# Performance work log

Measured on AMD Instinct MI355X. Metric: run time of the kernel, lower is better.

Reference implementation:

```python
import jax, jax.numpy as jnp
import numpy as np

D_MODEL = 1024
NUM_HEAD = 16
D_K = D_MODEL // NUM_HEAD


def setup_inputs() -> dict:
    key = jax.random.key(0)
    ks = jax.random.split(key, 11)
    B, S = 2, 2048
    s = 1.0 / np.sqrt(D_MODEL)
    return {
        "q": jax.random.normal(ks[0], (B, S, D_MODEL), jnp.float32),
        "k": jax.random.normal(ks[1], (B, S, D_MODEL), jnp.float32),
        "v": jax.random.normal(ks[2], (B, S, D_MODEL), jnp.float32),
        "Wq": jax.random.normal(ks[3], (D_MODEL, D_MODEL), jnp.float32) * s,
        "bq": jnp.zeros((D_MODEL,), jnp.float32),
        "Wk": jax.random.normal(ks[4], (D_MODEL, D_MODEL), jnp.float32) * s,
        "bk": jnp.zeros((D_MODEL,), jnp.float32),
        "Wv": jax.random.normal(ks[5], (D_MODEL, D_MODEL), jnp.float32) * s,
        "bv": jnp.zeros((D_MODEL,), jnp.float32),
        "Wo": jax.random.normal(ks[6], (D_MODEL, D_MODEL), jnp.float32) * s,
        "bo": jnp.zeros((D_MODEL,), jnp.float32),
    }


def _split_head(x, B):
    # [B, S, d_model] -> [B, H, S, d_k]
    S = x.shape[1]
    return x.reshape(B, S, NUM_HEAD, D_K).transpose(0, 2, 1, 3)


def reference(q, k, v, Wq, bq, Wk, bk, Wv, bv, Wo, bo):
    B = q.shape[0]
    qh = _split_head(q @ Wq + bq, B)  # [B,H,Sq,dk]
    kh = _split_head(k @ Wk + bk, B)  # [B,H,Sk,dk]
    vh = _split_head(v @ Wv + bv, B)  # [B,H,Sk,dk]
    scores = jnp.einsum("bhqd,bhkd->bhqk", qh, kh) / jnp.sqrt(
        jnp.asarray(D_K, qh.dtype)
    )
    attn = jax.nn.softmax(scores, axis=-1)
    out = jnp.einsum("bhqk,bhkd->bhqd", attn, vh)  # [B,H,Sq,dk]
    out = out.transpose(0, 2, 1, 3).reshape(B, -1, D_MODEL)
    return jax.nn.relu(out @ Wo + bo)
```

## Files before the change

kernel.cpp:

```cpp
#include <hip/hip_runtime.h>
#include <math.h>

#define SEQ 2048
#define NHD 16

typedef float f32x4 __attribute__((ext_vector_type(4), may_alias));
typedef _Float16 h16x8 __attribute__((ext_vector_type(8), may_alias));
typedef _Float16 h16x4 __attribute__((ext_vector_type(4), may_alias));

__device__ __forceinline__ void gl_lds16(const void* g, void* l) {
  __builtin_amdgcn_global_load_lds(
      (const __attribute__((address_space(1))) unsigned int*)g,
      (__attribute__((address_space(3))) unsigned int*)l, 16, 0, 0);
}

struct PrepArgs {
  const float* W[4];
  _Float16* T[4];
  const float* X[3];
  _Float16* H[3];
};

__global__ __launch_bounds__(256) void prep_k(PrepArgs a) {
  __shared__ float tile[64][65];
  const int blk = blockIdx.x;
  const int t = threadIdx.x;
  if (blk < 1024) {
    const int widx = blk >> 8, tl = blk & 255;
    const int nb = (tl & 15) * 64, kb = (tl >> 4) * 64;
    const float* __restrict__ W = a.W[widx];
    _Float16* __restrict__ T = a.T[widx];
    const int c = t & 63, r0 = t >> 6;
#pragma unroll
    for (int i = 0; i < 16; ++i) {
      const int r = i * 4 + r0;
      tile[r][c] = W[(size_t)(kb + r) * 1024 + nb + c];
    }
    __syncthreads();
#pragma unroll
    for (int i = 0; i < 16; ++i) {
      const int n = i * 4 + r0;
      T[(size_t)(nb + n) * 1024 + kb + c] = (_Float16)tile[c][n];
    }
  } else {
    const int b2 = blk - 1024;
    const int z = b2 >> 11, bx = b2 & 2047;
    const float* __restrict__ X = a.X[z];
    _Float16* __restrict__ H = a.H[z];
    const size_t i = ((size_t)bx * 256 + t) * 8;
    const f32x4 f0 = *(const f32x4*)(X + i);
    const f32x4 f1 = *(const f32x4*)(X + i + 4);
    const float fs[8] = {f0.x, f0.y, f0.z, f0.w, f1.x, f1.y, f1.z, f1.w};
    h16x8 o;
#pragma unroll
    for (int j = 0; j < 8; ++j) o[j] = (_Float16)fs[j];
    *(h16x8*)(H + i) = o;
  }
}

__global__ __launch_bounds__(256) void vtrans_k(const unsigned short* __restrict__ Vb,
                                                unsigned short* __restrict__ Vt) {
  __shared__ unsigned short tile[64][65];
  const int t = threadIdx.x;
  const int c = t & 63, r0 = t >> 6;
  const int s0 = blockIdx.x * 64;
  const int bh = blockIdx.y;
#pragma unroll
  for (int i = 0; i < 16; ++i) {
    const int r = i * 4 + r0;
    tile[r][c] = Vb[((size_t)bh * SEQ + s0 + r) * 64 + c];
  }
  __syncthreads();
#pragma unroll
  for (int i = 0; i < 16; ++i) {
    const int d = i * 4 + r0;
    const int sp = ((c & 15) * 4) + (c >> 4);
    Vt[((size_t)bh * 64 + d) * SEQ + s0 + sp] = tile[c][d];
  }
}

struct QKVArgs {
  const _Float16* A[3];
  const _Float16* Bt[3];
  const float* bias[3];
  _Float16* C[3];
};

__global__ __launch_bounds__(256, 4) void gemm_qkv_k(QKVArgs a) {
  __shared__ char smem[32768];
  const int dblk = blockIdx.x;
  const int z = dblk >> 8;
  const int rb = dblk & 255;
  const int n0 = ((rb >> 3) & 7) * 128;
  const int m0 = ((((rb >> 6) << 3) | (rb & 7))) * 128;
  const _Float16* __restrict__ A = a.A[z];
  const _Float16* __restrict__ Bt = a.Bt[z];
  const float* __restrict__ bias = a.bias[z];
  _Float16* __restrict__ C = a.C[z];

  const int t = threadIdx.x;
  const int l = t & 63, w = t >> 6;
  const int quad = l >> 4, l15 = l & 15;
  const int wm = w >> 1, wn = w & 1;

  auto stage = [&](int buf, int k0) {
#pragma unroll
    for (int it = 0; it < 2; ++it) {
      const int c = it * 4 + w;
      const int rr = c * 16 + l15;
      gl_lds16(A + (size_t)(m0 + rr) * 1024 + k0 + quad * 8,
               smem + buf * 16384 + c * 1024);
      gl_lds16(Bt + (size_t)(n0 + rr) * 1024 + k0 + quad * 8,
               smem + buf * 16384 + 8192 + c * 1024);
    }
  };

  const f32x4 z4 = {0.f, 0.f, 0.f, 0.f};
  f32x4 acc[4][4];
#pragma unroll
  for (int i = 0; i < 4; ++i)
#pragma unroll
    for (int j = 0; j < 4; ++j) acc[i][j] = z4;

  stage(0, 0);
  __syncthreads();
  int cur = 0;
  for (int k0 = 0; k0 < 1024; k0 += 32) {
    if (k0 + 32 < 1024) stage(cur ^ 1, k0 + 32);
    const h16x8* lds8 = (const h16x8*)(smem + cur * 16384);
    h16x8 af[4], bf[4];
#pragma unroll
    for (int i = 0; i < 4; ++i) {
      af[i] = lds8[(wm * 4 + i) * 64 + l];
      bf[i] = lds8[512 + (wn * 4 + i) * 64 + l];
    }
#pragma unroll
    for (int i = 0; i < 4; ++i)
#pragma unroll
      for (int j = 0; j < 4; ++j)
        acc[i][j] = __builtin_amdgcn_mfma_f32_16x16x32_f16(af[i], bf[j], acc[i][j], 0, 0, 0);
    __syncthreads();
    cur ^= 1;
  }
#pragma unroll
  for (int i = 0; i < 4; ++i)
#pragma unroll
    for (int j = 0; j < 4; ++j) {
      const int col = n0 + wn * 64 + j * 16 + l15;
      const float bv = bias[col];
#pragma unroll
      for (int r = 0; r < 4; ++r) {
        const int row = m0 + wm * 64 + i * 16 + quad * 4 + r;
        const int b = row >> 11, s = row & 2047;
        const int h = col >> 6, d = col & 63;
        C[((size_t)(b * NHD + h) * SEQ + s) * 64 + d] = (_Float16)(acc[i][j][r] + bv);
      }
    }
}

__global__ __launch_bounds__(256) void gemm_o_k(
    const _Float16* __restrict__ Op0, const _Float16* __restrict__ Op1,
    const float* __restrict__ Lp, const _Float16* __restrict__ Bt,
    const float* __restrict__ bias, float* __restrict__ Cf) {
  __shared__ char smem[40960];
  float* inv_lds = (float*)(smem + 32768);
  const int rb = blockIdx.x;
  const int n0 = ((rb >> 3) & 7) * 128;
  const int m0 = ((((rb >> 6) << 3) | (rb & 7))) * 128;
  const int t = threadIdx.x;
  const int l = t & 63, w = t >> 6;
  const int quad = l >> 4, l15 = l & 15;
  const int wm = w >> 1, wn = w & 1;
  const int arow0 = t >> 2, aq = t & 3;

#pragma unroll
  for (int e = t; e < 2048; e += 256) {
    const int rl = e >> 4, hh = e & 15;
    const int m = m0 + rl;
    const int b = m >> 11, s = m & 2047;
    const size_t li = (size_t)(b * NHD + hh) * 2048 + s;
    inv_lds[e] = 1.f / (Lp[li] + Lp[65536 + li]);
  }
  __syncthreads();

  auto stageB = [&](int buf, int k0) {
#pragma unroll
    for (int it = 0; it < 2; ++it) {
      const int c = it * 4 + w;
      const int rr = c * 16 + l15;
      gl_lds16(Bt + (size_t)(n0 + rr) * 1024 + k0 + quad * 8,
               smem + buf * 8192 + c * 1024);
    }
  };
  auto loadA = [&](int k0, h16x8 (&r0)[2], h16x8 (&r1)[2]) {
#pragma unroll
    for (int it = 0; it < 2; ++it) {
      const size_t off = (size_t)(m0 + it * 64 + arow0) * 1024 + k0 + aq * 8;
      r0[it] = *(const h16x8*)(Op0 + off);
      r1[it] = *(const h16x8*)(Op1 + off);
    }
  };
  auto writeA = [&](int buf, int k0, const h16x8 (&r0)[2], const h16x8 (&r1)[2]) {
    const int head = k0 >> 6;
    h16x8* alds = (h16x8*)(smem + 16384 + buf * 8192);
#pragma unroll
    for (int it = 0; it < 2; ++it) {
      const int row = it * 64 + arow0;
      const int slot = (row >> 4) * 64 + aq * 16 + ((row & 15) ^ (aq * 2));
      const float inv = inv_lds[row * 16 + head];
      h16x8 hv;
#pragma unroll
      for (int j = 0; j < 8; ++j)
        hv[j] = (_Float16)(((float)r0[it][j] + (float)r1[it][j]) * inv);
      alds[slot] = hv;
    }
  };

  const f32x4 z4 = {0.f, 0.f, 0.f, 0.f};
  f32x4 acc[4][4];
#pragma unroll
  for (int i = 0; i < 4; ++i)
#pragma unroll
    for (int j = 0; j < 4; ++j) acc[i][j] = z4;

  h16x8 a0r[2], a1r[2];
  loadA(0, a0r, a1r);
  stageB(0, 0);
  writeA(0, 0, a0r, a1r);
  __syncthreads();
  int cur = 0;
  for (int k0 = 0; k0 < 1024; k0 += 32) {
    const int nk = k0 + 32;
    if (nk < 1024) {
      loadA(nk, a0r, a1r);
      stageB(cur ^ 1, nk);
    }
    const h16x8* blds = (const h16x8*)(smem + cur * 8192);
    const h16x8* alds = (const h16x8*)(smem + 16384 + cur * 8192);
    h16x8 af[4], bf[4];
#pragma unroll
    for (int i = 0; i < 4; ++i) {
      af[i] = alds[(wm * 4 + i) * 64 + quad * 16 + (l15 ^ (quad * 2))];
      bf[i] = blds[(wn * 4 + i) * 64 + l];
    }
#pragma unroll
    for (int i = 0; i < 4; ++i)
#pragma unroll
      for (int j = 0; j < 4; ++j)
        acc[i][j] = __builtin_amdgcn_mfma_f32_16x16x32_f16(af[i], bf[j], acc[i][j], 0, 0, 0);
    if (nk < 1024) writeA(cur ^ 1, nk, a0r, a1r);
    __syncthreads();
    cur ^= 1;
  }
#pragma unroll
  for (int i = 0; i < 4; ++i)
#pragma unroll
    for (int j = 0; j < 4; ++j) {
      const int col = n0 + wn * 64 + j * 16 + l15;
      const float bv = bias[col];
#pragma unroll
      for (int r = 0; r < 4; ++r) {
        const int row = m0 + wm * 64 + i * 16 + quad * 4 + r;
        Cf[(size_t)row * 1024 + col] = fmaxf(acc[i][j][r] + bv, 0.f);
      }
    }
}

__global__ __launch_bounds__(256, 4) void attn_k(
    const _Float16* __restrict__ Qf, const _Float16* __restrict__ Kf,
    const _Float16* __restrict__ Vtp,
    _Float16* __restrict__ Op0, _Float16* __restrict__ Op1,
    float* __restrict__ Lp) {
  __shared__ char smem[34816];
  h16x8* lds8 = (h16x8*)smem;
  const int dblk = blockIdx.x;
  const int comb = ((dblk >> 7) << 3) | (dblk & 7);
  const int q0 = ((dblk >> 3) & 15) * 128;
  const int bh = comb >> 1;
  const int kz = comb & 1;
  const int t = threadIdx.x;
  const int l = t & 63, w = t >> 6;
  const int quad = l >> 4, l15 = l & 15;
  const int b = bh >> 4, h = bh & 15;

  const _Float16* Kb = Kf + (size_t)bh * SEQ * 64;
  const _Float16* Vtb = Vtp + (size_t)bh * 64 * SEQ;

  h16x8 qf[2][2];
#pragma unroll
  for (int mi = 0; mi < 2; ++mi) {
    const size_t qb = ((size_t)bh * SEQ + q0 + w * 32 + mi * 16 + l15) * 64;
#pragma unroll
    for (int ks = 0; ks < 2; ++ks)
      qf[mi][ks] = *(const h16x8*)&Qf[qb + ks * 32 + quad * 8];
  }
  const f32x4 z4 = {0.f, 0.f, 0.f, 0.f};
  f32x4 oacc[2][4], lacc[2];
#pragma unroll
  for (int mi = 0; mi < 2; ++mi) {
    lacc[mi] = z4;
#pragma unroll
    for (int i = 0; i < 4; ++i) oacc[mi][i] = z4;
  }
  h16x8 ones;
#pragma unroll
  for (int j = 0; j < 8; ++j) ones[j] = (_Float16)1.0f;

  const int kbeg = kz * 1024;
  for (int k0 = kbeg; k0 < kbeg + 1024; k0 += 64) {
#pragma unroll
    for (int it = 0; it < 2; ++it) {
      const int c = it * 4 + w;
      const int kd = (c >> 1) * 16 + l15;
      const int off2 = (c & 1) * 32 + quad * 8;
      gl_lds16(Kb + (size_t)(k0 + kd) * 64 + off2, smem + c * 1024);
      gl_lds16(Vtb + (size_t)kd * SEQ + k0 + off2, smem + 8192 + c * 1024);
    }
    __syncthreads();

    {
      h16x8 kfr[4][2];
#pragma unroll
      for (int nt = 0; nt < 4; ++nt)
#pragma unroll
        for (int ks = 0; ks < 2; ++ks) kfr[nt][ks] = lds8[(nt * 2 + ks) * 64 + l];

#pragma unroll
      for (int mi = 0; mi < 2; ++mi) {
        f32x4 sacc[4];
#pragma unroll
        for (int nt = 0; nt < 4; ++nt) {
          f32x4 s = z4;
          s = __builtin_amdgcn_mfma_f32_16x16x32_f16(qf[mi][0], kfr[nt][0], s, 0, 0, 0);
          s = __builtin_amdgcn_mfma_f32_16x16x32_f16(qf[mi][1], kfr[nt][1], s, 0, 0, 0);
          sacc[nt] = s;
        }
        char* pb = smem + 16384 + (w * 2 + mi) * 2304;
#pragma unroll
        for (int r = 0; r < 4; ++r) {
          h16x4 pk;
#pragma unroll
          for (int nt = 0; nt < 4; ++nt)
            pk[nt] = (_Float16)__expf(sacc[nt][r] * 0.125f);
          *(h16x4*)(pb + (quad * 4 + r) * 144 + l15 * 8) = pk;
        }
      }
    }
    __asm__ __volatile__("" ::: "memory");

    {
      h16x8 vfr[4][2];
#pragma unroll
      for (int nt = 0; nt < 4; ++nt)
#pragma unroll
        for (int ks = 0; ks < 2; ++ks) vfr[nt][ks] = lds8[512 + (nt * 2 + ks) * 64 + l];

#pragma unroll
      for (int mi = 0; mi < 2; ++mi) {
        char* pb = smem + 16384 + (w * 2 + mi) * 2304;
        const h16x8 pf0 = *(const h16x8*)(pb + l15 * 144 + quad * 16);
        const h16x8 pf1 = *(const h16x8*)(pb + l15 * 144 + 64 + quad * 16);
        lacc[mi] = __builtin_amdgcn_mfma_f32_16x16x32_f16(pf0, ones, lacc[mi], 0, 0, 0);
        lacc[mi] = __builtin_amdgcn_mfma_f32_16x16x32_f16(pf1, ones, lacc[mi], 0, 0, 0);
#pragma unroll
        for (int nt = 0; nt < 4; ++nt) {
          oacc[mi][nt] = __builtin_amdgcn_mfma_f32_16x16x32_f16(pf0, vfr[nt][0], oacc[mi][nt], 0, 0, 0);
          oacc[mi][nt] = __builtin_amdgcn_mfma_f32_16x16x32_f16(pf1, vfr[nt][1], oacc[mi][nt], 0, 0, 0);
        }
      }
    }
    __syncthreads();
  }

  _Float16* __restrict__ Op = kz ? Op1 : Op0;
#pragma unroll
  for (int mi = 0; mi < 2; ++mi)
#pragma unroll
    for (int nt = 0; nt < 4; ++nt)
#pragma unroll
      for (int r = 0; r < 4; ++r) {
        const size_t tok = (size_t)b * SEQ + q0 + w * 32 + mi * 16 + quad * 4 + r;
        Op[tok * 1024 + h * 64 + nt * 16 + l15] = (_Float16)oacc[mi][nt][r];
      }
  if (l15 == 0) {
#pragma unroll
    for (int mi = 0; mi < 2; ++mi)
#pragma unroll
      for (int r = 0; r < 4; ++r) {
        const int row = q0 + w * 32 + mi * 16 + quad * 4 + r;
        Lp[(size_t)kz * 65536 + bh * 2048 + row] = lacc[mi][r];
      }
  }
}

extern "C" void kernel_launch(void* const* d_in, const int* in_sizes, int n_in,
                              void* d_out, int out_size, void* d_ws, size_t ws_size,
                              hipStream_t stream) {
  const float* q = (const float*)d_in[0];
  const float* k = (const float*)d_in[1];
  const float* v = (const float*)d_in[2];
  const float* Wq = (const float*)d_in[3];
  const float* bq = (const float*)d_in[4];
  const float* Wk = (const float*)d_in[5];
  const float* bk = (const float*)d_in[6];
  const float* Wv = (const float*)d_in[7];
  const float* bv = (const float*)d_in[8];
  const float* Wo = (const float*)d_in[9];
  const float* bo = (const float*)d_in[10];

  char* W8 = (char*)d_ws;
  const size_t MB = 1024 * 1024;
  auto F = [&](size_t off) { return (_Float16*)(W8 + off); };
  _Float16* wt[4] = {F(0), F(2 * MB), F(4 * MB), F(6 * MB)};
  _Float16* qf = F(8 * MB);
  _Float16* kf = F(16 * MB);
  _Float16* vf = F(24 * MB);
  _Float16* Qf = F(32 * MB);
  _Float16* Kf = F(40 * MB);
  _Float16* Vb = F(48 * MB);
  _Float16* Vt = F(56 * MB);
  _Float16* Op0 = F(8 * MB);
  _Float16* Op1 = F(16 * MB);
  float* Lp = (float*)(W8 + 64 * MB);

  const dim3 blk(256);

  PrepArgs pa;
  pa.W[0] = Wq; pa.W[1] = Wk; pa.W[2] = Wv; pa.W[3] = Wo;
  pa.T[0] = wt[0]; pa.T[1] = wt[1]; pa.T[2] = wt[2]; pa.T[3] = wt[3];
  pa.X[0] = q; pa.X[1] = k; pa.X[2] = v;
  pa.H[0] = qf; pa.H[1] = kf; pa.H[2] = vf;
  prep_k<<<dim3(7168), blk, 0, stream>>>(pa);

  QKVArgs qa;
  qa.A[0] = qf; qa.A[1] = kf; qa.A[2] = vf;
  qa.Bt[0] = wt[0]; qa.Bt[1] = wt[1]; qa.Bt[2] = wt[2];
  qa.bias[0] = bq; qa.bias[1] = bk; qa.bias[2] = bv;
  qa.C[0] = Qf; qa.C[1] = Kf; qa.C[2] = Vb;
  gemm_qkv_k<<<dim3(768), blk, 0, stream>>>(qa);

  vtrans_k<<<dim3(32, 32), blk, 0, stream>>>((const unsigned short*)Vb,
                                             (unsigned short*)Vt);
  attn_k<<<dim3(1024), blk, 0, stream>>>(Qf, Kf, Vt, Op0, Op1, Lp);
  gemm_o_k<<<dim3(256), blk, 0, stream>>>(Op0, Op1, Lp, wt[3], bo, (float*)d_out);
}
```

Measured before the change: 254.4 us.

## Enlarge QKV GEMM tiles to 256x256 with 512 threads and swizzled LDS

Rewrites the fused QKV projection GEMM to use 256x256 output tiles with 8 waves per block, a K-step of 64, and 128 KB of double-buffered LDS. An XOR swizzle is applied to the LDS layout to avoid bank conflicts, and explicit vmcnt waits plus raw barriers replace __syncthreads. The goal is more data reuse per LDS load and fewer global loads per MFMA. In exchange only 192 blocks are launched, which may underfill the GPU's CUs, and each thread holds a larger accumulator set, so register pressure rises.

```diff
diff --git a/kernel.cpp b/kernel.cpp
--- a/kernel.cpp
+++ b/kernel.cpp
@@ -86,13 +86,13 @@
   _Float16* C[3];
 };
 
-__global__ __launch_bounds__(256, 4) void gemm_qkv_k(QKVArgs a) {
-  __shared__ char smem[32768];
+__global__ __launch_bounds__(512, 2) void gemm_qkv_k(QKVArgs a) {
+  __shared__ __align__(16) char smem[131072];
   const int dblk = blockIdx.x;
-  const int z = dblk >> 8;
-  const int rb = dblk & 255;
-  const int n0 = ((rb >> 3) & 7) * 128;
-  const int m0 = ((((rb >> 6) << 3) | (rb & 7))) * 128;
+  const int z = dblk >> 6;
+  const int rb = dblk & 63;
+  const int m0 = (rb >> 2) * 256;
+  const int n0 = (rb & 3) * 256;
   const _Float16* __restrict__ A = a.A[z];
   const _Float16* __restrict__ Bt = a.Bt[z];
   const float* __restrict__ bias = a.bias[z];
@@ -101,59 +101,86 @@
   const int t = threadIdx.x;
   const int l = t & 63, w = t >> 6;
   const int quad = l >> 4, l15 = l & 15;
-  const int wm = w >> 1, wn = w & 1;
-
-  auto stage = [&](int buf, int k0) {
-#pragma unroll
-    for (int it = 0; it < 2; ++it) {
-      const int c = it * 4 + w;
-      const int rr = c * 16 + l15;
-      gl_lds16(A + (size_t)(m0 + rr) * 1024 + k0 + quad * 8,
-               smem + buf * 16384 + c * 1024);
-      gl_lds16(Bt + (size_t)(n0 + rr) * 1024 + k0 + quad * 8,
-               smem + buf * 16384 + 8192 + c * 1024);
+  const int wm = w >> 2, wn = w & 3;
+
+  const int srow = t >> 3;
+  const int sslot = (t & 7) ^ (srow & 7);
+  size_t goffA[4], goffB[4];
+#pragma unroll
+  for (int j = 0; j < 4; ++j) {
+    goffA[j] = (size_t)(m0 + j * 64 + srow) * 1024 + sslot * 8;
+    goffB[j] = (size_t)(n0 + j * 64 + srow) * 1024 + sslot * 8;
+  }
+
+  auto stage = [&](int buf, int kt) {
+    const int k0 = kt * 64;
+    char* base = smem + buf * 65536;
+#pragma unroll
+    for (int j = 0; j < 4; ++j) {
+      gl_lds16(A + goffA[j] + k0, base + j * 8192 + w * 1024);
+      gl_lds16(Bt + goffB[j] + k0, base + 32768 + j * 8192 + w * 1024);
     }
   };
 
   const f32x4 z4 = {0.f, 0.f, 0.f, 0.f};
-  f32x4 acc[4][4];
-#pragma unroll
-  for (int i = 0; i < 4; ++i)
+  f32x4 acc[8][4];
+#pragma unroll
+  for (int i = 0; i < 8; ++i)
 #pragma unroll
     for (int j = 0; j < 4; ++j) acc[i][j] = z4;
 
+  const int xr = l15 & 7;
+
   stage(0, 0);
-  __syncthreads();
-  int cur = 0;
-  for (int k0 = 0; k0 < 1024; k0 += 32) {
-    if (k0 + 32 < 1024) stage(cur ^ 1, k0 + 32);
-    const h16x8* lds8 = (const h16x8*)(smem + cur * 16384);
-    h16x8 af[4], bf[4];
-#pragma unroll
-    for (int i = 0; i < 4; ++i) {
-      af[i] = lds8[(wm * 4 + i) * 64 + l];
-      bf[i] = lds8[512 + (wn * 4 + i) * 64 + l];
-    }
-#pragma unroll
-    for (int i = 0; i < 4; ++i)
-#pragma unroll
-      for (int j = 0; j < 4; ++j)
-        acc[i][j] = __builtin_amdgcn_mfma_f32_16x16x32_f16(af[i], bf[j], acc[i][j], 0, 0, 0);
-    __syncthreads();
-    cur ^= 1;
-  }
-#pragma unroll
-  for (int i = 0; i < 4; ++i)
-#pragma unroll
-    for (int j = 0; j < 4; ++j) {
-      const int col = n0 + wn * 64 + j * 16 + l15;
+  for (int kt = 0; kt < 16; ++kt) {
+    const int cur = kt & 1;
+    if (kt < 15) {
+      stage(cur ^ 1, kt + 1);
+      asm volatile("s_waitcnt vmcnt(8)" ::: "memory");
+    } else {
+      asm volatile("s_waitcnt vmcnt(0)" ::: "memory");
+    }
+    __builtin_amdgcn_sched_barrier(0);
+    __builtin_amdgcn_s_barrier();
+
+    const char* base = smem + cur * 65536;
+    h16x8 bf[4][2];
+#pragma unroll
+    for (int nj = 0; nj < 4; ++nj) {
+      const int rowB = wn * 64 + nj * 16 + l15;
+#pragma unroll
+      for (int h = 0; h < 2; ++h) {
+        const int sl = (h * 4 + quad) ^ xr;
+        bf[nj][h] = *(const h16x8*)(base + 32768 + rowB * 128 + sl * 16);
+      }
+    }
+#pragma unroll
+    for (int mi = 0; mi < 8; ++mi) {
+      const int rowA = wm * 128 + mi * 16 + l15;
+      const h16x8 af0 = *(const h16x8*)(base + rowA * 128 + ((quad ^ xr) * 16));
+      const h16x8 af1 = *(const h16x8*)(base + rowA * 128 + (((4 + quad) ^ xr) * 16));
+#pragma unroll
+      for (int nj = 0; nj < 4; ++nj) {
+        acc[mi][nj] = __builtin_amdgcn_mfma_f32_16x16x32_f16(af0, bf[nj][0], acc[mi][nj], 0, 0, 0);
+        acc[mi][nj] = __builtin_amdgcn_mfma_f32_16x16x32_f16(af1, bf[nj][1], acc[mi][nj], 0, 0, 0);
+      }
+    }
+    __builtin_amdgcn_sched_barrier(0);
+    __builtin_amdgcn_s_barrier();
+  }
+
+#pragma unroll
+  for (int mi = 0; mi < 8; ++mi)
+#pragma unroll
+    for (int nj = 0; nj < 4; ++nj) {
+      const int col = n0 + wn * 64 + nj * 16 + l15;
       const float bv = bias[col];
 #pragma unroll
       for (int r = 0; r < 4; ++r) {
-        const int row = m0 + wm * 64 + i * 16 + quad * 4 + r;
+        const int row = m0 + wm * 128 + mi * 16 + quad * 4 + r;
         const int b = row >> 11, s = row & 2047;
         const int h = col >> 6, d = col & 63;
-        C[((size_t)(b * NHD + h) * SEQ + s) * 64 + d] = (_Float16)(acc[i][j][r] + bv);
+        C[((size_t)(b * NHD + h) * SEQ + s) * 64 + d] = (_Float16)(acc[mi][nj][r] + bv);
       }
     }
 }
@@ -437,7 +464,7 @@
   qa.Bt[0] = wt[0]; qa.Bt[1] = wt[1]; qa.Bt[2] = wt[2];
   qa.bias[0] = bq; qa.bias[1] = bk; qa.bias[2] = bv;
   qa.C[0] = Qf; qa.C[1] = Kf; qa.C[2] = Vb;
-  gemm_qkv_k<<<dim3(768), blk, 0, stream>>>(qa);
+  gemm_qkv_k<<<dim3(192), dim3(512), 0, stream>>>(qa);
 
   vtrans_k<<<dim3(32, 32), blk, 0, stream>>>((const unsigned short*)Vb,
                                              (unsigned short*)Vt);
```

Result: faster. 237.2 us (-6.8%).
